# Performance work log

Measured on AMD Instinct MI355X. Metric: run time of the kernel, lower is better.

Reference implementation:

```python
import jax, jax.numpy as jnp
import numpy as np

C = 128      # in channels
CO = 64      # out channels
G = 32       # group-norm groups
RES_IN = 32  # input resolution
RES_OUT = 64 # subdivided resolution
N = 20000    # active input voxels
EPS = 1e-5


def setup_inputs() -> dict:
    key = jax.random.key(0)
    ks = jax.random.split(key, 12)
    # unique active voxel coords at RES_IN (batch index 0, single instance)
    rng = np.random.default_rng(0)
    flat = rng.choice(RES_IN ** 3, size=N, replace=False)
    xyz = np.stack([flat // (RES_IN * RES_IN), (flat // RES_IN) % RES_IN, flat % RES_IN], axis=1)
    x_coords = jnp.asarray(np.concatenate([np.zeros((N, 1), np.int32), xyz.astype(np.int32)], axis=1))
    x_feats = jax.random.normal(ks[0], (N, C), dtype=jnp.float32)
    gn1_g = 1.0 + 0.1 * jax.random.normal(ks[1], (C,), dtype=jnp.float32)
    gn1_b = 0.1 * jax.random.normal(ks[2], (C,), dtype=jnp.float32)
    W1 = 0.05 * jax.random.normal(ks[3], (3, 3, 3, C, CO), dtype=jnp.float32)
    b1 = 0.01 * jax.random.normal(ks[4], (CO,), dtype=jnp.float32)
    gn2_g = 1.0 + 0.1 * jax.random.normal(ks[5], (CO,), dtype=jnp.float32)
    gn2_b = 0.1 * jax.random.normal(ks[6], (CO,), dtype=jnp.float32)
    W2 = 0.05 * jax.random.normal(ks[7], (3, 3, 3, CO, CO), dtype=jnp.float32)  # zero_module in source; random here to exercise math
    b2 = 0.01 * jax.random.normal(ks[8], (CO,), dtype=jnp.float32)
    Ws = 0.05 * jax.random.normal(ks[9], (C, CO), dtype=jnp.float32)   # 1x1 skip conv
    bs = 0.01 * jax.random.normal(ks[10], (CO,), dtype=jnp.float32)
    return dict(x_feats=x_feats, x_coords=x_coords, gn1_g=gn1_g, gn1_b=gn1_b,
                W1=W1, b1=b1, gn2_g=gn2_g, gn2_b=gn2_b, W2=W2, b2=b2, Ws=Ws, bs=bs)


def group_norm(f, g, b):
    # single-instance sparse group norm: stats per group over all points
    n, c = f.shape
    x = f.reshape(n, G, c // G)
    mu = jnp.mean(x, axis=(0, 2), keepdims=True)
    var = jnp.mean((x - mu) ** 2, axis=(0, 2), keepdims=True)
    return ((x - mu) * jax.lax.rsqrt(var + EPS)).reshape(n, c) * g + b


def subdivide(coords, feats):
    n = coords.shape[0]
    offs = jnp.stack(jnp.meshgrid(jnp.arange(2), jnp.arange(2), jnp.arange(2), indexing='ij'), -1).reshape(8, 3)
    xyz = coords[:, None, 1:] * 2 + offs[None].astype(coords.dtype)          # [n,8,3]
    bidx = jnp.broadcast_to(coords[:, None, :1], (n, 8, 1))
    new_coords = jnp.concatenate([bidx, xyz], axis=-1).reshape(n * 8, 4)
    return new_coords, jnp.repeat(feats, 8, axis=0)


def subm_conv3(coords, feats, W, b):
    # submanifold 3x3x3 sparse conv: scatter to padded dense grid, gather 27 neighbors per active site
    cin = feats.shape[1]
    grid = jnp.zeros((RES_OUT + 2, RES_OUT + 2, RES_OUT + 2, cin), feats.dtype)
    grid = grid.at[coords[:, 1] + 1, coords[:, 2] + 1, coords[:, 3] + 1].set(feats)
    acc = jnp.zeros((feats.shape[0], W.shape[-1]), feats.dtype)
    for i in range(3):
        for j in range(3):
            for k in range(3):
                nb = grid[coords[:, 1] + i, coords[:, 2] + j, coords[:, 3] + k]  # [n, cin]
                acc = acc + nb @ W[i, j, k]
    return acc + b


def reference(x_feats, x_coords, gn1_g, gn1_b, W1, b1, gn2_g, gn2_b, W2, b2, Ws, bs):
    h = jax.nn.silu(group_norm(x_feats, gn1_g, gn1_b))
    hc, hf = subdivide(x_coords, h)
    _, xf = subdivide(x_coords, x_feats)
    hf = subm_conv3(hc, hf, W1, b1)
    hf = jax.nn.silu(group_norm(hf, gn2_g, gn2_b))
    hf = subm_conv3(hc, hf, W2, b2)
    out = hf + (xf @ Ws + bs)  # residual + 1x1 skip conv (out_channels != channels)
    return out
```

## Files before the change

kernel.cpp:

```cpp
#include <hip/hip_runtime.h>
#include <hip/hip_bf16.h>
#include <math.h>

#define N_PTS 20000
#define C_IN 128
#define C_OUT 64
#define M_PTS (N_PTS*8)
#define EPS 1e-5f

typedef __attribute__((ext_vector_type(8))) short short8;
typedef __attribute__((ext_vector_type(4))) float float4v;

__device__ __forceinline__ ushort f2bf(float f){
    unsigned int i = __float_as_uint(f);
    unsigned int r = i + 0x7fffu + ((i >> 16) & 1u);
    return (ushort)(r >> 16);
}
__device__ __forceinline__ float bf2f(ushort u){ return __uint_as_float(((unsigned int)u) << 16); }
__device__ __forceinline__ float silu(float z){ return z / (1.f + expf(-z)); }


__global__ void __launch_bounds__(256) prep_kernel(
    const float* __restrict__ W1, const float* __restrict__ W2,
    ushort* __restrict__ Wt1, ushort* __restrict__ Wt2,
    int* __restrict__ pg, ushort* __restrict__ h, ushort* __restrict__ h2,
    const float* __restrict__ x, float* __restrict__ stats)
{
    const int b = blockIdx.x, tid = threadIdx.x;
    if (b < 864){
        int idx = b * 256 + tid;
        int j = idx & 7, l = (idx >> 3) & 63, nb = (idx >> 9) & 3, kb = (idx >> 11) & 3, t = idx >> 13;
        int ci = kb * 32 + (l >> 4) * 8 + j, co = nb * 16 + (l & 15);
        Wt1[idx] = f2bf(W1[(t * C_IN + ci) * 64 + co]);
    } else if (b < 1296){
        int idx = (b - 864) * 256 + tid;
        int j = idx & 7, l = (idx >> 3) & 63, nb = (idx >> 9) & 3, kb = (idx >> 11) & 1, t = idx >> 12;
        int ci = kb * 32 + (l >> 4) * 8 + j, co = nb * 16 + (l & 15);
        Wt2[idx] = f2bf(W2[(t * C_OUT + ci) * 64 + co]);
    } else if (b < 1424){
        int i = (b - 1296) * 256 + tid;
        pg[i] = -1;
        if (b == 1296){
            if (tid < C_IN) h[(size_t)N_PTS * C_IN + tid] = 0;
            if (tid < C_OUT) h2[(size_t)M_PTS * C_OUT + tid] = 0;
        }
    } else {
        __shared__ float ls[64];
        if (tid < 64) ls[tid] = 0.f;
        __syncthreads();
        const int g = tid & 31;
        const int r0 = (b - 1424) * 8 + (tid >> 5);
        float sum = 0.f, sq = 0.f;
        for (int r = r0; r < N_PTS; r += 4096){
            float4 v = *(const float4*)(x + (size_t)r * C_IN + g * 4);
            sum += v.x + v.y + v.z + v.w;
            sq  += v.x*v.x + v.y*v.y + v.z*v.z + v.w*v.w;
        }
        atomicAdd(&ls[g], sum);
        atomicAdd(&ls[32 + g], sq);
        __syncthreads();
        if (tid < 64) atomicAdd(&stats[tid], ls[tid]);
    }
}

__global__ void __launch_bounds__(256) mid_kernel(
    const int* __restrict__ cds, int* __restrict__ pg,
    const float* __restrict__ x, const float* __restrict__ stats,
    const float* __restrict__ g1, const float* __restrict__ b1, ushort* __restrict__ h,
    const float* __restrict__ Wsk, const float* __restrict__ bsk, float* __restrict__ s)
{
    __shared__ float w[C_IN * C_OUT];
    const int b = blockIdx.x, tid = threadIdx.x;
    if (b < 79){
        int i = b * 256 + tid;
        if (i < N_PTS){
            const int* cd = cds + i * 4;
            pg[(cd[1] * 32 + cd[2]) * 32 + cd[3]] = i;
        }
    } else if (b < 2579){
        int i = ((b - 79) * 256 + tid) * 4;
        int c0 = i & (C_IN - 1);
        int g = c0 >> 2;
        float mu = stats[g] * (1.0f / (N_PTS * 4.0f));
        float var = stats[32 + g] * (1.0f / (N_PTS * 4.0f)) - mu * mu;
        float rs = rsqrtf(var + EPS);
        float4 v = *(const float4*)(x + i);
        ushort4 o;
        o.x = f2bf(silu((v.x - mu) * rs * g1[c0+0] + b1[c0+0]));
        o.y = f2bf(silu((v.y - mu) * rs * g1[c0+1] + b1[c0+1]));
        o.z = f2bf(silu((v.z - mu) * rs * g1[c0+2] + b1[c0+2]));
        o.w = f2bf(silu((v.w - mu) * rs * g1[c0+3] + b1[c0+3]));
        *(ushort4*)(h + i) = o;
    } else {
        for (int j = tid; j < C_IN * C_OUT; j += 256) w[j] = Wsk[j];
        __syncthreads();
        int co = tid & 63, pr = tid >> 6;
        int p = (b - 2579) * 4 + pr;
        const float* xr = x + (size_t)p * C_IN;
        float a = bsk[co];
        for (int cb = 0; cb < C_IN; cb += 4){
            float4 v = *(const float4*)(xr + cb);
            a += v.x * w[(cb+0)*64+co] + v.y * w[(cb+1)*64+co]
               + v.z * w[(cb+2)*64+co] + v.w * w[(cb+3)*64+co];
        }
        s[(size_t)p * C_OUT + co] = a;
    }
}

template<int CIN, int CHILD>
__global__ void __launch_bounds__(64, 3) conv_direct(
    const ushort* __restrict__ feat, const int* __restrict__ pg,
    const int* __restrict__ coords, const ushort* __restrict__ Wt,
    const float* __restrict__ bias, const float* __restrict__ skip,
    ushort* __restrict__ hf1_bf, float* __restrict__ out, float* __restrict__ statsAcc)
{
    constexpr int KB = CIN / 32;
    constexpr int ZROW = CHILD ? (8 * N_PTS) : N_PTS;
    const int l = threadIdx.x;
    const int r16 = l & 15, qd = l >> 4;
    const int mb = blockIdx.x * 64;

    int cx0, cy0, cz0;
    {
        int m = mb + l, p = m >> 3, o = m & 7;
        cx0 = 2 * coords[p*4+1] + ((o >> 2) & 1);
        cy0 = 2 * coords[p*4+2] + ((o >> 1) & 1);
        cz0 = 2 * coords[p*4+3] + (o & 1);
    }

    int rows[27];
#pragma unroll
    for (int t = 0; t < 27; t++){
        const int dx = t / 9 - 1, dy = (t / 3) % 3 - 1, dz = t % 3 - 1;
        const int cx = cx0 + dx, cy = cy0 + dy, cz = cz0 + dz;
        int row = ZROW;
        if ((unsigned)(cx | cy | cz) < 64u){
            int pidx = pg[(cx >> 1) * 1024 + (cy >> 1) * 32 + (cz >> 1)];
            if (pidx >= 0)
                row = CHILD ? pidx * 8 + (((cx & 1) << 2) | ((cy & 1) << 1) | (cz & 1))
                            : pidx;
        }
        rows[t] = row;
    }

    float4v acc[4][4];
#pragma unroll
    for (int rb = 0; rb < 4; rb++)
#pragma unroll
        for (int nb = 0; nb < 4; nb++)
#pragma unroll
            for (int rg = 0; rg < 4; rg++) acc[rb][nb][rg] = 0.f;

#pragma unroll
    for (int t = 0; t < 27; t++){
        int fr0 = __shfl(rows[t],      r16, 64);
        int fr1 = __shfl(rows[t], 16 + r16, 64);
        int fr2 = __shfl(rows[t], 32 + r16, 64);
        int fr3 = __shfl(rows[t], 48 + r16, 64);
        const ushort* a0 = feat + (size_t)fr0 * CIN + qd * 8;
        const ushort* a1 = feat + (size_t)fr1 * CIN + qd * 8;
        const ushort* a2 = feat + (size_t)fr2 * CIN + qd * 8;
        const ushort* a3 = feat + (size_t)fr3 * CIN + qd * 8;
        const ushort* wt = Wt + (size_t)t * (KB * 2048) + l * 8;
#pragma unroll
        for (int kb = 0; kb < KB; kb++){
            short8 b0 = *(const short8*)(wt + (kb*4+0)*512);
            short8 b1 = *(const short8*)(wt + (kb*4+1)*512);
            short8 b2 = *(const short8*)(wt + (kb*4+2)*512);
            short8 b3 = *(const short8*)(wt + (kb*4+3)*512);
            short8 av0 = *(const short8*)(a0 + kb*32);
            short8 av1 = *(const short8*)(a1 + kb*32);
            short8 av2 = *(const short8*)(a2 + kb*32);
            short8 av3 = *(const short8*)(a3 + kb*32);
            acc[0][0] = __builtin_amdgcn_mfma_f32_16x16x32_bf16(av0, b0, acc[0][0], 0, 0, 0);
            acc[0][1] = __builtin_amdgcn_mfma_f32_16x16x32_bf16(av0, b1, acc[0][1], 0, 0, 0);
            acc[0][2] = __builtin_amdgcn_mfma_f32_16x16x32_bf16(av0, b2, acc[0][2], 0, 0, 0);
            acc[0][3] = __builtin_amdgcn_mfma_f32_16x16x32_bf16(av0, b3, acc[0][3], 0, 0, 0);
            acc[1][0] = __builtin_amdgcn_mfma_f32_16x16x32_bf16(av1, b0, acc[1][0], 0, 0, 0);
            acc[1][1] = __builtin_amdgcn_mfma_f32_16x16x32_bf16(av1, b1, acc[1][1], 0, 0, 0);
            acc[1][2] = __builtin_amdgcn_mfma_f32_16x16x32_bf16(av1, b2, acc[1][2], 0, 0, 0);
            acc[1][3] = __builtin_amdgcn_mfma_f32_16x16x32_bf16(av1, b3, acc[1][3], 0, 0, 0);
            acc[2][0] = __builtin_amdgcn_mfma_f32_16x16x32_bf16(av2, b0, acc[2][0], 0, 0, 0);
            acc[2][1] = __builtin_amdgcn_mfma_f32_16x16x32_bf16(av2, b1, acc[2][1], 0, 0, 0);
            acc[2][2] = __builtin_amdgcn_mfma_f32_16x16x32_bf16(av2, b2, acc[2][2], 0, 0, 0);
            acc[2][3] = __builtin_amdgcn_mfma_f32_16x16x32_bf16(av2, b3, acc[2][3], 0, 0, 0);
            acc[3][0] = __builtin_amdgcn_mfma_f32_16x16x32_bf16(av3, b0, acc[3][0], 0, 0, 0);
            acc[3][1] = __builtin_amdgcn_mfma_f32_16x16x32_bf16(av3, b1, acc[3][1], 0, 0, 0);
            acc[3][2] = __builtin_amdgcn_mfma_f32_16x16x32_bf16(av3, b2, acc[3][2], 0, 0, 0);
            acc[3][3] = __builtin_amdgcn_mfma_f32_16x16x32_bf16(av3, b3, acc[3][3], 0, 0, 0);
        }
    }

    float bsv[4] = { bias[r16], bias[16 + r16], bias[32 + r16], bias[48 + r16] };
    if (!CHILD){
        float ps[4] = {0,0,0,0}, pq[4] = {0,0,0,0};
#pragma unroll
        for (int rb = 0; rb < 4; rb++)
#pragma unroll
            for (int nb = 0; nb < 4; nb++)
#pragma unroll
                for (int rg = 0; rg < 4; rg++){
                    int mm = mb + rb * 16 + qd * 4 + rg;
                    float v = acc[rb][nb][rg] + bsv[nb];
                    hf1_bf[(size_t)mm * 64 + nb * 16 + r16] = f2bf(v);
                    ps[nb] += v; pq[nb] += v * v;
                }
#pragma unroll
        for (int nb = 0; nb < 4; nb++){
            float s1 = ps[nb], s2 = pq[nb];
            s1 += __shfl_xor(s1, 16, 64); s2 += __shfl_xor(s2, 16, 64);
            s1 += __shfl_xor(s1, 32, 64); s2 += __shfl_xor(s2, 32, 64);
            if (qd == 0){
                atomicAdd(&statsAcc[64 + nb * 16 + r16], s1);
                atomicAdd(&statsAcc[128 + nb * 16 + r16], s2);
            }
        }
    } else {
#pragma unroll
        for (int rb = 0; rb < 4; rb++)
#pragma unroll
            for (int rg = 0; rg < 4; rg++){
                int mm = mb + rb * 16 + qd * 4 + rg;
                const float* sk = skip + (size_t)(mm >> 3) * 64;
#pragma unroll
                for (int nb = 0; nb < 4; nb++){
                    int co = nb * 16 + r16;
                    out[(size_t)mm * 64 + co] = acc[rb][nb][rg] + bsv[nb] + sk[co];
                }
            }
    }
}

__global__ void __launch_bounds__(256) h2_kernel(
    const ushort* __restrict__ hf1, const float* __restrict__ stats,
    const float* __restrict__ gg, const float* __restrict__ gb, ushort* __restrict__ h2)
{
    int i = (blockIdx.x * 256 + threadIdx.x) * 4;
    if (i >= M_PTS * C_OUT) return;
    int c0 = i & (C_OUT - 1);
    const float inv = 1.0f / (M_PTS * 2.0f);
    float muA = (stats[64 + c0] + stats[64 + c0 + 1]) * inv;
    float vA  = (stats[128 + c0] + stats[128 + c0 + 1]) * inv - muA * muA;
    float rsA = rsqrtf(vA + EPS);
    float muB = (stats[64 + c0 + 2] + stats[64 + c0 + 3]) * inv;
    float vB  = (stats[128 + c0 + 2] + stats[128 + c0 + 3]) * inv - muB * muB;
    float rsB = rsqrtf(vB + EPS);
    ushort4 u = *(const ushort4*)(hf1 + i);
    ushort4 o;
    o.x = f2bf(silu((bf2f(u.x) - muA) * rsA * gg[c0+0] + gb[c0+0]));
    o.y = f2bf(silu((bf2f(u.y) - muA) * rsA * gg[c0+1] + gb[c0+1]));
    o.z = f2bf(silu((bf2f(u.z) - muB) * rsB * gg[c0+2] + gb[c0+2]));
    o.w = f2bf(silu((bf2f(u.w) - muB) * rsB * gg[c0+3] + gb[c0+3]));
    *(ushort4*)(h2 + i) = o;
}

extern "C" void kernel_launch(void* const* d_in, const int* in_sizes, int n_in,
                              void* d_out, int out_size, void* d_ws, size_t ws_size,
                              hipStream_t stream){
    const float* x   = (const float*)d_in[0];
    const int*   cds = (const int*)  d_in[1];
    const float* g1  = (const float*)d_in[2];
    const float* b1  = (const float*)d_in[3];
    const float* W1  = (const float*)d_in[4];
    const float* bb1 = (const float*)d_in[5];
    const float* g2  = (const float*)d_in[6];
    const float* b2  = (const float*)d_in[7];
    const float* W2  = (const float*)d_in[8];
    const float* bb2 = (const float*)d_in[9];
    const float* Wsk = (const float*)d_in[10];
    const float* bsk = (const float*)d_in[11];
    float* out = (float*)d_out;
    char* ws = (char*)d_ws;

    float*  stats = (float*) (ws);
    int*    pg    = (int*)   (ws + 1024);
    ushort* h     = (ushort*)(ws + 132096);
    ushort* h2    = (ushort*)(ws + 5252352);
    float*  s     = (float*) (ws + 25732480);
    ushort* Wt1   = (ushort*)(ws + 30852480);
    ushort* Wt2   = (ushort*)(ws + 31294848);

    hipMemsetAsync(stats, 0, 192 * sizeof(float), stream);
    prep_kernel<<<1936, 256, 0, stream>>>(W1, W2, Wt1, Wt2, pg, h, h2, x, stats);
    mid_kernel<<<7579, 256, 0, stream>>>(cds, pg, x, stats, g1, b1, h, Wsk, bsk, s);
    conv_direct<C_IN, 0><<<2500, 64, 0, stream>>>(h, pg, cds, Wt1, bb1, nullptr,
                                                  (ushort*)d_out, nullptr, stats);
    h2_kernel<<<12500, 256, 0, stream>>>((const ushort*)d_out, stats, g2, b2, h2);
    conv_direct<C_OUT, 1><<<2500, 64, 0, stream>>>(h2, pg, cds, Wt2, bb2, s,
                                                   nullptr, out, nullptr);
}
```

Baseline: 405.1 us.

## Split conv taps across two waves per block with LDS reduction

Each conv block now runs two wavefronts, each computing the MFMA accumulation over roughly half of the 27 neighbor taps for the same 64 output rows. The second wave writes its partial accumulators to shared memory, and the first wave adds them before the existing epilogue. This doubles the number of resident waves to hide gather and load latency in the latency-bound sparse conv. The cost is a 16KB shared buffer per block, a block-level sync, and the reduction traffic.

```diff
diff --git a/kernel.cpp b/kernel.cpp
--- a/kernel.cpp
+++ b/kernel.cpp
@@ -107,30 +107,18 @@
     }
 }
 
-template<int CIN, int CHILD>
-__global__ void __launch_bounds__(64, 3) conv_direct(
+template<int CIN, int CHILD, int TBEG, int TEND>
+__device__ __forceinline__ void conv_taps(
     const ushort* __restrict__ feat, const int* __restrict__ pg,
-    const int* __restrict__ coords, const ushort* __restrict__ Wt,
-    const float* __restrict__ bias, const float* __restrict__ skip,
-    ushort* __restrict__ hf1_bf, float* __restrict__ out, float* __restrict__ statsAcc)
+    const ushort* __restrict__ Wt,
+    int cx0, int cy0, int cz0, int l, int r16, int qd,
+    float4v acc[16])
 {
     constexpr int KB = CIN / 32;
     constexpr int ZROW = CHILD ? (8 * N_PTS) : N_PTS;
-    const int l = threadIdx.x;
-    const int r16 = l & 15, qd = l >> 4;
-    const int mb = blockIdx.x * 64;
-
-    int cx0, cy0, cz0;
-    {
-        int m = mb + l, p = m >> 3, o = m & 7;
-        cx0 = 2 * coords[p*4+1] + ((o >> 2) & 1);
-        cy0 = 2 * coords[p*4+2] + ((o >> 1) & 1);
-        cz0 = 2 * coords[p*4+3] + (o & 1);
-    }
-
-    int rows[27];
-#pragma unroll
-    for (int t = 0; t < 27; t++){
+    int rows[TEND - TBEG];
+#pragma unroll
+    for (int t = TBEG; t < TEND; t++){
         const int dx = t / 9 - 1, dy = (t / 3) % 3 - 1, dz = t % 3 - 1;
         const int cx = cx0 + dx, cy = cy0 + dy, cz = cz0 + dz;
         int row = ZROW;
@@ -140,23 +128,14 @@
                 row = CHILD ? pidx * 8 + (((cx & 1) << 2) | ((cy & 1) << 1) | (cz & 1))
                             : pidx;
         }
-        rows[t] = row;
-    }
-
-    float4v acc[4][4];
-#pragma unroll
-    for (int rb = 0; rb < 4; rb++)
-#pragma unroll
-        for (int nb = 0; nb < 4; nb++)
-#pragma unroll
-            for (int rg = 0; rg < 4; rg++) acc[rb][nb][rg] = 0.f;
-
-#pragma unroll
-    for (int t = 0; t < 27; t++){
-        int fr0 = __shfl(rows[t],      r16, 64);
-        int fr1 = __shfl(rows[t], 16 + r16, 64);
-        int fr2 = __shfl(rows[t], 32 + r16, 64);
-        int fr3 = __shfl(rows[t], 48 + r16, 64);
+        rows[t - TBEG] = row;
+    }
+#pragma unroll
+    for (int t = TBEG; t < TEND; t++){
+        int fr0 = __shfl(rows[t - TBEG],      r16, 64);
+        int fr1 = __shfl(rows[t - TBEG], 16 + r16, 64);
+        int fr2 = __shfl(rows[t - TBEG], 32 + r16, 64);
+        int fr3 = __shfl(rows[t - TBEG], 48 + r16, 64);
         const ushort* a0 = feat + (size_t)fr0 * CIN + qd * 8;
         const ushort* a1 = feat + (size_t)fr1 * CIN + qd * 8;
         const ushort* a2 = feat + (size_t)fr2 * CIN + qd * 8;
@@ -172,24 +151,64 @@
             short8 av1 = *(const short8*)(a1 + kb*32);
             short8 av2 = *(const short8*)(a2 + kb*32);
             short8 av3 = *(const short8*)(a3 + kb*32);
-            acc[0][0] = __builtin_amdgcn_mfma_f32_16x16x32_bf16(av0, b0, acc[0][0], 0, 0, 0);
-            acc[0][1] = __builtin_amdgcn_mfma_f32_16x16x32_bf16(av0, b1, acc[0][1], 0, 0, 0);
-            acc[0][2] = __builtin_amdgcn_mfma_f32_16x16x32_bf16(av0, b2, acc[0][2], 0, 0, 0);
-            acc[0][3] = __builtin_amdgcn_mfma_f32_16x16x32_bf16(av0, b3, acc[0][3], 0, 0, 0);
-            acc[1][0] = __builtin_amdgcn_mfma_f32_16x16x32_bf16(av1, b0, acc[1][0], 0, 0, 0);
-            acc[1][1] = __builtin_amdgcn_mfma_f32_16x16x32_bf16(av1, b1, acc[1][1], 0, 0, 0);
-            acc[1][2] = __builtin_amdgcn_mfma_f32_16x16x32_bf16(av1, b2, acc[1][2], 0, 0, 0);
-            acc[1][3] = __builtin_amdgcn_mfma_f32_16x16x32_bf16(av1, b3, acc[1][3], 0, 0, 0);
-            acc[2][0] = __builtin_amdgcn_mfma_f32_16x16x32_bf16(av2, b0, acc[2][0], 0, 0, 0);
-            acc[2][1] = __builtin_amdgcn_mfma_f32_16x16x32_bf16(av2, b1, acc[2][1], 0, 0, 0);
-            acc[2][2] = __builtin_amdgcn_mfma_f32_16x16x32_bf16(av2, b2, acc[2][2], 0, 0, 0);
-            acc[2][3] = __builtin_amdgcn_mfma_f32_16x16x32_bf16(av2, b3, acc[2][3], 0, 0, 0);
-            acc[3][0] = __builtin_amdgcn_mfma_f32_16x16x32_bf16(av3, b0, acc[3][0], 0, 0, 0);
-            acc[3][1] = __builtin_amdgcn_mfma_f32_16x16x32_bf16(av3, b1, acc[3][1], 0, 0, 0);
-            acc[3][2] = __builtin_amdgcn_mfma_f32_16x16x32_bf16(av3, b2, acc[3][2], 0, 0, 0);
-            acc[3][3] = __builtin_amdgcn_mfma_f32_16x16x32_bf16(av3, b3, acc[3][3], 0, 0, 0);
-        }
-    }
+            acc[0]  = __builtin_amdgcn_mfma_f32_16x16x32_bf16(av0, b0, acc[0],  0, 0, 0);
+            acc[1]  = __builtin_amdgcn_mfma_f32_16x16x32_bf16(av0, b1, acc[1],  0, 0, 0);
+            acc[2]  = __builtin_amdgcn_mfma_f32_16x16x32_bf16(av0, b2, acc[2],  0, 0, 0);
+            acc[3]  = __builtin_amdgcn_mfma_f32_16x16x32_bf16(av0, b3, acc[3],  0, 0, 0);
+            acc[4]  = __builtin_amdgcn_mfma_f32_16x16x32_bf16(av1, b0, acc[4],  0, 0, 0);
+            acc[5]  = __builtin_amdgcn_mfma_f32_16x16x32_bf16(av1, b1, acc[5],  0, 0, 0);
+            acc[6]  = __builtin_amdgcn_mfma_f32_16x16x32_bf16(av1, b2, acc[6],  0, 0, 0);
+            acc[7]  = __builtin_amdgcn_mfma_f32_16x16x32_bf16(av1, b3, acc[7],  0, 0, 0);
+            acc[8]  = __builtin_amdgcn_mfma_f32_16x16x32_bf16(av2, b0, acc[8],  0, 0, 0);
+            acc[9]  = __builtin_amdgcn_mfma_f32_16x16x32_bf16(av2, b1, acc[9],  0, 0, 0);
+            acc[10] = __builtin_amdgcn_mfma_f32_16x16x32_bf16(av2, b2, acc[10], 0, 0, 0);
+            acc[11] = __builtin_amdgcn_mfma_f32_16x16x32_bf16(av2, b3, acc[11], 0, 0, 0);
+            acc[12] = __builtin_amdgcn_mfma_f32_16x16x32_bf16(av3, b0, acc[12], 0, 0, 0);
+            acc[13] = __builtin_amdgcn_mfma_f32_16x16x32_bf16(av3, b1, acc[13], 0, 0, 0);
+            acc[14] = __builtin_amdgcn_mfma_f32_16x16x32_bf16(av3, b2, acc[14], 0, 0, 0);
+            acc[15] = __builtin_amdgcn_mfma_f32_16x16x32_bf16(av3, b3, acc[15], 0, 0, 0);
+        }
+    }
+}
+
+template<int CIN, int CHILD>
+__global__ void __launch_bounds__(128, 4) conv_direct(
+    const ushort* __restrict__ feat, const int* __restrict__ pg,
+    const int* __restrict__ coords, const ushort* __restrict__ Wt,
+    const float* __restrict__ bias, const float* __restrict__ skip,
+    ushort* __restrict__ hf1_bf, float* __restrict__ out, float* __restrict__ statsAcc)
+{
+    __shared__ float4v lacc[16][64];
+    const int tid = threadIdx.x;
+    const int wid = tid >> 6, l = tid & 63;
+    const int r16 = l & 15, qd = l >> 4;
+    const int mb = blockIdx.x * 64;
+
+    int cx0, cy0, cz0;
+    {
+        int m = mb + l, p = m >> 3, o = m & 7;
+        cx0 = 2 * coords[p*4+1] + ((o >> 2) & 1);
+        cy0 = 2 * coords[p*4+2] + ((o >> 1) & 1);
+        cz0 = 2 * coords[p*4+3] + (o & 1);
+    }
+
+    float4v acc[16];
+#pragma unroll
+    for (int c = 0; c < 16; c++) acc[c] = 0.f;
+
+    if (wid == 0)
+        conv_taps<CIN, CHILD, 0, 14>(feat, pg, Wt, cx0, cy0, cz0, l, r16, qd, acc);
+    else
+        conv_taps<CIN, CHILD, 14, 27>(feat, pg, Wt, cx0, cy0, cz0, l, r16, qd, acc);
+
+    if (wid == 1){
+#pragma unroll
+        for (int c = 0; c < 16; c++) lacc[c][l] = acc[c];
+    }
+    __syncthreads();
+    if (wid == 1) return;
+#pragma unroll
+    for (int c = 0; c < 16; c++) acc[c] += lacc[c][l];
 
     float bsv[4] = { bias[r16], bias[16 + r16], bias[32 + r16], bias[48 + r16] };
     if (!CHILD){
@@ -201,7 +220,7 @@
 #pragma unroll
                 for (int rg = 0; rg < 4; rg++){
                     int mm = mb + rb * 16 + qd * 4 + rg;
-                    float v = acc[rb][nb][rg] + bsv[nb];
+                    float v = acc[rb * 4 + nb][rg] + bsv[nb];
                     hf1_bf[(size_t)mm * 64 + nb * 16 + r16] = f2bf(v);
                     ps[nb] += v; pq[nb] += v * v;
                 }
@@ -225,7 +244,7 @@
 #pragma unroll
                 for (int nb = 0; nb < 4; nb++){
                     int co = nb * 16 + r16;
-                    out[(size_t)mm * 64 + co] = acc[rb][nb][rg] + bsv[nb] + sk[co];
+                    out[(size_t)mm * 64 + co] = acc[rb * 4 + nb][rg] + bsv[nb] + sk[co];
                 }
             }
     }
@@ -283,9 +302,9 @@
     hipMemsetAsync(stats, 0, 192 * sizeof(float), stream);
     prep_kernel<<<1936, 256, 0, stream>>>(W1, W2, Wt1, Wt2, pg, h, h2, x, stats);
     mid_kernel<<<7579, 256, 0, stream>>>(cds, pg, x, stats, g1, b1, h, Wsk, bsk, s);
-    conv_direct<C_IN, 0><<<2500, 64, 0, stream>>>(h, pg, cds, Wt1, bb1, nullptr,
-                                                  (ushort*)d_out, nullptr, stats);
+    conv_direct<C_IN, 0><<<2500, 128, 0, stream>>>(h, pg, cds, Wt1, bb1, nullptr,
+                                                   (ushort*)d_out, nullptr, stats);
     h2_kernel<<<12500, 256, 0, stream>>>((const ushort*)d_out, stats, g2, b2, h2);
-    conv_direct<C_OUT, 1><<<2500, 64, 0, stream>>>(h2, pg, cds, Wt2, bb2, s,
-                                                   nullptr, out, nullptr);
-}
+    conv_direct<C_OUT, 1><<<2500, 128, 0, stream>>>(h2, pg, cds, Wt2, bb2, s,
+                                                    nullptr, out, nullptr);
+}
```

Measured after the change: 451.1 us. 1.11x slower.
